# Kernel optimization log

Hardware: AMD Instinct MI355X
Metric: run time of the kernel (lower is better)

Reference implementation:

```python
import jax, jax.numpy as jnp
import numpy as np

K = 3  # Chebyshev filter size (max_view)


def avwgcn(X, E, weights_pool, bias_pool):
    """Adaptive node-wise graph conv. X: [B,N,C_in], E: [N,D]."""
    N = E.shape[0]
    # adaptive adjacency: softmax over rows of relu(E E^T)
    supports = jax.nn.softmax(jax.nn.relu(E @ E.T), axis=1)  # [N,N]
    support_set = [jnp.eye(N, dtype=X.dtype), supports]
    for _ in range(2, K):  # Chebyshev recursion
        support_set.append(2.0 * supports @ support_set[-1] - support_set[-2])
    S = jnp.stack(support_set, axis=0)  # [K,N,N]
    W = jnp.einsum('nd,dkio->nkio', E, weights_pool)  # per-node weights [N,K,Ci,Co]
    bias = E @ bias_pool  # [N,Co]
    XG = jnp.einsum('knm,bmc->bnkc', S, X)  # [B,N,K,Ci]
    return jnp.einsum('bnki,nkio->bno', XG, W) + bias  # [B,N,Co]


def setup_inputs() -> dict:
    key = jax.random.key(0)
    ks = jax.random.split(key, 5)
    B, N, Cin, Cout, D = 32, 4096, 2, 64, 10
    Ci = Cin + Cout  # 66
    X = jax.random.normal(ks[0], (B, N, Cin), dtype=jnp.float32)
    H = jnp.zeros((B, N, Cout), dtype=jnp.float32)
    E = jax.random.normal(ks[1], (N, D), dtype=jnp.float32)
    W_gate = jax.random.normal(ks[2], (D, K, Ci, 2 * Cout), dtype=jnp.float32) * 0.1
    b_gate = jnp.zeros((D, 2 * Cout), dtype=jnp.float32)
    W_update = jax.random.normal(ks[3], (D, K, Ci, Cout), dtype=jnp.float32) * 0.1
    b_update = jnp.zeros((D, Cout), dtype=jnp.float32)
    return {"X": X, "H": H, "E": E, "W_gate": W_gate, "b_gate": b_gate,
            "W_update": W_update, "b_update": b_update}


def reference(X, H, E, W_gate, b_gate, W_update, b_update):
    Cout = H.shape[-1]
    XH = jnp.concatenate([X, H], axis=-1)  # [B,N,Cin+Cout]
    ZR = jax.nn.sigmoid(avwgcn(XH, E, W_gate, b_gate))  # [B,N,2*Cout]
    Z, R = ZR[..., :Cout], ZR[..., Cout:]
    C = jnp.concatenate([X, Z * H], axis=-1)
    HC = jnp.tanh(avwgcn(C, E, W_update, b_update))
    return R * H + (1.0 - R) * HC
```

## Files before the change

### kernel.cpp

```cpp
#include <hip/hip_runtime.h>
#include <math.h>

#define N_NODES 4096
#define BATCH   32
#define D_EMB   10
#define CIN     2
#define COUT    64
#define CI      66
#define KSUP    3
#define NCOLS   2112
#define NPAD    2176
#define LDT     4096

#define KSEC    72
#define KI_REAL 216
#define KILD    232
#define OCH     (32 * KILD)
#define WROW_G  (128 * KILD)
#define WROW_U  (64 * KILD)
#define WGT2_R  (WROW_G + WROW_U)

typedef _Float16 half_t;
typedef __attribute__((ext_vector_type(8))) _Float16 f16x8;
typedef __attribute__((ext_vector_type(4))) _Float16 f16x4;
typedef __attribute__((ext_vector_type(2))) _Float16 f16x2;
typedef __attribute__((ext_vector_type(4))) float f32x4;

union u32h2 { unsigned u; f16x2 h; };

struct __attribute__((packed, aligned(4))) uint4_u4 { uint4 v; };
__device__ __forceinline__ f16x8 loadu8h(const half_t* p) {
  union { uint4 u; f16x8 h; } r;
  r.u = ((const uint4_u4*)p)->v;
  return r.h;
}

__device__ __forceinline__ float fast_sigmoid(float x) { return 1.f / (1.f + __expf(-x)); }
__device__ __forceinline__ float fast_tanh(float x) { return 1.f - 2.f / (__expf(2.f * x) + 1.f); }

__device__ __forceinline__ void gld_lds16(const half_t* g, half_t* l) {
  __builtin_amdgcn_global_load_lds(
      (const __attribute__((address_space(1))) void*)g,
      (__attribute__((address_space(3))) void*)l, 16, 0, 0);
}

__global__ __launch_bounds__(256) void k_softmax_p(const float* __restrict__ E,
                                                   half_t* __restrict__ Pb) {
  const int n = blockIdx.x;
  const int tid = threadIdx.x;
  __shared__ float En[D_EMB];
  __shared__ float ms[256], ss[256];
  if (tid < D_EMB) En[tid] = E[n * D_EMB + tid];
  __syncthreads();
  float en[D_EMB];
#pragma unroll
  for (int d = 0; d < D_EMB; ++d) en[d] = En[d];

  float val[16];
  float m = -1e30f, s = 0.f;
#pragma unroll
  for (int it = 0; it < 16; ++it) {
    const int c = tid + it * 256;
    const float* Ec = E + c * D_EMB;
    float v = 0.f;
#pragma unroll
    for (int d = 0; d < D_EMB; ++d) v += en[d] * Ec[d];
    v = fmaxf(v, 0.f);
    val[it] = v;
    if (v > m) { s *= __expf(m - v); m = v; }
    s += __expf(v - m);
  }
  ms[tid] = m; ss[tid] = s;
  __syncthreads();
  for (int off = 128; off > 0; off >>= 1) {
    if (tid < off) {
      float m2 = ms[tid + off], s2 = ss[tid + off];
      float m1 = ms[tid], s1 = ss[tid];
      float mm = fmaxf(m1, m2);
      ms[tid] = mm;
      ss[tid] = s1 * __expf(m1 - mm) + s2 * __expf(m2 - mm);
    }
    __syncthreads();
  }
  const float M = ms[0];
  const float inv = 1.f / ss[0];
  half_t* Pr = Pb + (size_t)n * N_NODES;
#pragma unroll
  for (int it = 0; it < 16; ++it)
    Pr[tid + it * 256] = (half_t)(__expf(val[it] - M) * inv);
}

__global__ __launch_bounds__(256) void k_build_v0(const float* __restrict__ X,
                                                  const float* __restrict__ H,
                                                  half_t* __restrict__ Vt,
                                                  half_t* __restrict__ Vn,
                                                  half_t* __restrict__ Cbn) {
  __shared__ half_t T[64][69];
  const int tid = threadIdx.x;
  const int ct = blockIdx.x * 64;
  const int mt = blockIdx.y * 64;
  const int r0 = tid >> 4;
  const int c4 = (tid & 15) * 4;
#pragma unroll
  for (int it = 0; it < 4; ++it) {
    const int r = r0 + it * 16;
    const int m = mt + r;
    half_t hv[4];
#pragma unroll
    for (int j = 0; j < 4; ++j) {
      const int col = ct + c4 + j;
      const int b = col / CI;
      const int c = col - b * CI;
      float v;
      if (c < CIN) v = X[((size_t)b * N_NODES + m) * CIN + c];
      else         v = H[((size_t)b * N_NODES + m) * COUT + (c - CIN)];
      hv[j] = (half_t)v;
      T[r][c4 + j] = hv[j];
      if (c < CIN) Cbn[(size_t)m * NPAD + col] = hv[j];
    }
    f16x4 v4 = {hv[0], hv[1], hv[2], hv[3]};
    *(f16x4*)&Vn[(size_t)m * NPAD + ct + c4] = v4;
  }
  __syncthreads();
#pragma unroll
  for (int it = 0; it < 4; ++it) {
    const int cc = r0 + it * 16;
    const int m4 = c4;
    f16x4 v = {T[m4 + 0][cc], T[m4 + 1][cc], T[m4 + 2][cc], T[m4 + 3][cc]};
    *(f16x4*)&Vt[(size_t)(ct + cc) * LDT + mt + m4] = v;
  }
}

__device__ __forceinline__ void gemm_compute_tile(const half_t* __restrict__ Lb,
                                                  int wm, int wn, int fofs,
                                                  f32x4 (&acc)[4][2]) {
  f16x8 a[4], b[2];
#pragma unroll
  for (int i = 0; i < 4; ++i)
    a[i] = *(const f16x8*)&Lb[((wm >> 4) + i) * 512 + fofs];
#pragma unroll
  for (int j = 0; j < 2; ++j)
    b[j] = *(const f16x8*)&Lb[4096 + ((wn >> 4) + j) * 512 + fofs];
  __builtin_amdgcn_s_setprio(1);
#pragma unroll
  for (int i = 0; i < 4; ++i)
#pragma unroll
    for (int j = 0; j < 2; ++j)
      acc[i][j] = __builtin_amdgcn_mfma_f32_16x16x32_f16(a[i], b[j], acc[i][j], 0, 0, 0);
  __builtin_amdgcn_s_setprio(0);
}

__global__ __launch_bounds__(512) void k_gemm_f16(const half_t* __restrict__ A,
                                                  const half_t* __restrict__ Bt,
                                                  half_t* __restrict__ Cn,
                                                  half_t* __restrict__ Ct) {
  __shared__ half_t LB[4][8192];
  const int tid = threadIdx.x;
  const int lane = tid & 63;
  const int wave = tid >> 6;

  int flat = blockIdx.y * 17 + blockIdx.x;
  flat = (flat & 7) * 68 + (flat >> 3);
  const int bx = flat % 17;
  const int by = flat / 17;

  const int wm = (wave >> 2) * 64;
  const int wn = (wave & 3) * 32;
  const int rb = by * 128;
  const int cb = bx * 128;

  const int srow = lane >> 2;
  const int skg = (((lane & 3) + ((lane >> 3) & 3)) & 3) * 8;
  const half_t* ga0 = A + (size_t)(rb + wave * 16 + srow) * N_NODES + skg;
  const half_t* gb0 = Bt + (size_t)(cb + wave * 16 + srow) * LDT + skg;
  const int lA0 = wave * 512;
  const int lB0 = 4096 + wave * 512;

  const int fr = lane & 15;
  const int fg = lane >> 4;
  const int fofs = (4 * fr + ((fg - (fr >> 1)) & 3)) * 8;

  f32x4 acc[4][2] = {};

#define STAGE_T(buf, kk) do { half_t* Lp = LB[(buf)]; \
    gld_lds16(ga0 + (kk), Lp + lA0); gld_lds16(gb0 + (kk), Lp + lB0); } while (0)

  STAGE_T(0, 0);
  STAGE_T(1, 32);
  STAGE_T(2, 64);

  for (int t = 0; t < 124; t += 4) {
    asm volatile("s_waitcnt vmcnt(4)\n\ts_barrier" ::: "memory");
    STAGE_T(3, (t + 3) * 32);
    gemm_compute_tile(LB[0], wm, wn, fofs, acc);

    asm volatile("s_waitcnt vmcnt(4)\n\ts_barrier" ::: "memory");
    STAGE_T(0, (t + 4) * 32);
    gemm_compute_tile(LB[1], wm, wn, fofs, acc);

    asm volatile("s_waitcnt vmcnt(4)\n\ts_barrier" ::: "memory");
    STAGE_T(1, (t + 5) * 32);
    gemm_compute_tile(LB[2], wm, wn, fofs, acc);

    asm volatile("s_waitcnt vmcnt(4)\n\ts_barrier" ::: "memory");
    STAGE_T(2, (t + 6) * 32);
    gemm_compute_tile(LB[3], wm, wn, fofs, acc);
  }
  asm volatile("s_waitcnt vmcnt(4)\n\ts_barrier" ::: "memory");
  STAGE_T(3, 127 * 32);
  gemm_compute_tile(LB[0], wm, wn, fofs, acc);
  asm volatile("s_waitcnt vmcnt(4)\n\ts_barrier" ::: "memory");
  gemm_compute_tile(LB[1], wm, wn, fofs, acc);
  asm volatile("s_waitcnt vmcnt(2)\n\ts_barrier" ::: "memory");
  gemm_compute_tile(LB[2], wm, wn, fofs, acc);
  asm volatile("s_waitcnt vmcnt(0)\n\ts_barrier" ::: "memory");
  gemm_compute_tile(LB[3], wm, wn, fofs, acc);
#undef STAGE_T

  const int en = lane & 15;
  const int em = (lane >> 4) * 4;
#pragma unroll
  for (int i = 0; i < 4; ++i) {
#pragma unroll
    for (int j = 0; j < 2; ++j) {
      const int m0 = rb + wm + i * 16 + em;
      const int n = cb + wn + j * 16 + en;
      half_t h0 = (half_t)acc[i][j][0];
      half_t h1 = (half_t)acc[i][j][1];
      half_t h2 = (half_t)acc[i][j][2];
      half_t h3 = (half_t)acc[i][j][3];
      if (Ct) {
        f16x4 t4 = {h0, h1, h2, h3};
        *(f16x4*)&Ct[(size_t)n * LDT + m0] = t4;
      }
      Cn[(size_t)(m0 + 0) * NPAD + n] = h0;
      Cn[(size_t)(m0 + 1) * NPAD + n] = h1;
      Cn[(size_t)(m0 + 2) * NPAD + n] = h2;
      Cn[(size_t)(m0 + 3) * NPAD + n] = h3;
    }
  }
}

__global__ __launch_bounds__(256) void k_tr(const half_t* __restrict__ Cbn,
                                            half_t* __restrict__ Ct) {
  __shared__ half_t T[64][69];
  const int tid = threadIdx.x;
  const int cb = blockIdx.x * 64;
  const int mb = blockIdx.y * 64;
  const int c4 = (tid & 15) * 4;
  const int r0 = tid >> 4;
#pragma unroll
  for (int it = 0; it < 4; ++it) {
    const int r = r0 + it * 16;
    f16x4 v = *(const f16x4*)&Cbn[(size_t)(mb + r) * NPAD + cb + c4];
    T[r][c4 + 0] = v[0];
    T[r][c4 + 1] = v[1];
    T[r][c4 + 2] = v[2];
    T[r][c4 + 3] = v[3];
  }
  __syncthreads();
#pragma unroll
  for (int it = 0; it < 4; ++it) {
    const int c2 = r0 + it * 16;
    const int m4 = c4;
    f16x4 v = {T[m4 + 0][c2], T[m4 + 1][c2], T[m4 + 2][c2], T[m4 + 3][c2]};
    *(f16x4*)&Ct[(size_t)(cb + c2) * LDT + mb + m4] = v;
  }
}

__global__ __launch_bounds__(256) void k_wgt2(const float* __restrict__ Wg,
                                              const float* __restrict__ Wu,
                                              unsigned* __restrict__ WT2) {
  const int r = blockIdx.x * 256 + threadIdx.x;
  if (r >= WGT2_R) return;
  const float* pool;
  int o, ki, ostr;
  if (r < WROW_G) { o = r / KILD; ki = r % KILD; pool = Wg; ostr = 128; }
  else { int r2 = r - WROW_G; o = r2 / KILD; ki = r2 % KILD; pool = Wu; ostr = 64; }
  const int k = ki / KSEC;
  const int i = ki - k * KSEC;
#pragma unroll
  for (int dp = 0; dp < 5; ++dp) {
    u32h2 v; v.h = f16x2{(half_t)0.f, (half_t)0.f};
    if (ki < KI_REAL && i < CI) {
      v.h[0] = (half_t)pool[(((size_t)(2 * dp) * KSUP + k) * CI + i) * ostr + o];
      v.h[1] = (half_t)pool[(((size_t)(2 * dp + 1) * KSUP + k) * CI + i) * ostr + o];
    }
    WT2[(size_t)dp * WGT2_R + r] = v.u;
  }
}

__device__ __forceinline__ void stage_xg4(const half_t* __restrict__ v0b,
                                          const half_t* __restrict__ g1b,
                                          const half_t* __restrict__ g2b,
                                          half_t* __restrict__ xg,
                                          int n0, int tid, int nthr) {
  for (int w = tid; w < 4 * 288; w += nthr) {
    const int nd = w / 288;
    const int rem = w - nd * 288;
    const int b = rem / 9;
    const int oct = rem - b * 9;
    const size_t src = (size_t)(n0 + nd) * NPAD + b * CI;
    half_t* row = xg + nd * OCH + b * KILD;
    const half_t* pv = v0b + src;
    const half_t* pg1 = g1b + src;
    const half_t* pg2 = g2b + src;
    if (oct < 8) {
      const f16x8 v0 = loadu8h(pv + oct * 8);
      const f16x8 g1 = loadu8h(pg1 + oct * 8);
      const f16x8 g2 = loadu8h(pg2 + oct * 8);
      const f16x8 x2 = g2 + g2 - v0;
      *(f16x8*)&row[oct * 8] = v0;
      *(f16x8*)&row[KSEC + oct * 8] = g1;
      *(f16x8*)&row[2 * KSEC + oct * 8] = x2;
    } else {
      u32h2 tv, tg1, tg2;
      tv.u = *(const unsigned*)(pv + 64);
      tg1.u = *(const unsigned*)(pg1 + 64);
      tg2.u = *(const unsigned*)(pg2 + 64);
      f16x8 v0 = {}, g1 = {}, x2 = {};
      v0[0] = tv.h[0]; v0[1] = tv.h[1];
      g1[0] = tg1.h[0]; g1[1] = tg1.h[1];
      x2[0] = tg2.h[0] + tg2.h[0] - tv.h[0];
      x2[1] = tg2.h[1] + tg2.h[1] - tv.h[1];
      *(f16x8*)&row[64] = v0;
      *(f16x8*)&row[KSEC + 64] = g1;
      *(f16x8*)&row[2 * KSEC + 64] = x2;
    }
  }
  for (int w = tid; w < 4 * 64; w += nthr) {
    const int nd = w >> 6;
    const int z = w & 63;
    const f16x8 zz = {};
    *(f16x8*)&xg[nd * OCH + (z >> 1) * KILD + KI_REAL + (z & 1) * 8] = zz;
  }
}

__global__ __launch_bounds__(512) void k_gate_t(const half_t* __restrict__ Vn,
                                                const half_t* __restrict__ G1n,
                                                const half_t* __restrict__ G2n,
                                                const unsigned* __restrict__ WT2,
                                                const float* __restrict__ E,
                                                const float* __restrict__ bg,
                                                const float* __restrict__ H,
                                                half_t* __restrict__ Cbn,
                                                half_t* __restrict__ Rb) {
  const int n0 = blockIdx.x * 4;
  const int tid = threadIdx.x;
  const int lane = tid & 63;
  const int wave = tid >> 6;
  __shared__ half_t S[4 * OCH];
  __shared__ float biasl[4][128];

  f16x2 e2p[4][5];
#pragma unroll
  for (int nd = 0; nd < 4; ++nd)
#pragma unroll
    for (int dp = 0; dp < 5; ++dp) {
      e2p[nd][dp][0] = (half_t)E[(n0 + nd) * D_EMB + 2 * dp];
      e2p[nd][dp][1] = (half_t)E[(n0 + nd) * D_EMB + 2 * dp + 1];
    }

  {
    const int nn = tid >> 7;
    const int o = tid & 127;
    float s = 0.f;
#pragma unroll
    for (int d = 0; d < D_EMB; ++d) s += E[(n0 + nn) * D_EMB + d] * bg[d * 128 + o];
    biasl[nn][o] = s;
  }
  stage_xg4(Vn, G1n, G2n, S, n0, tid, 512);
  __syncthreads();

  const int fr = lane & 15;
  const int fk = (lane >> 4) * 8;
  const int en = lane & 15;
  const int em = (lane >> 4) * 4;
  const int node = wave & 3;
  const int bh = wave >> 2;
  const int nn = n0 + node;

  f16x8 af[7];
#pragma unroll
  for (int ks = 0; ks < 7; ++ks)
    af[ks] = *(const f16x8*)&S[node * OCH + (bh * 16 + fr) * KILD + ks * 32 + fk];
  __syncthreads();

#pragma unroll
  for (int p = 0; p < 4; ++p) {
    if (p > 0) __syncthreads();
    for (int base = tid * 8; base < OCH; base += 4096) {
      float a[4][8] = {};
#pragma unroll
      for (int dp = 0; dp < 5; ++dp) {
        const unsigned* wrow = WT2 + (size_t)dp * WGT2_R + p * OCH + base;
        uint4 wa = *(const uint4*)wrow;
        uint4 wb = *(const uint4*)(wrow + 4);
        u32h2 c0, c1, c2, c3;
        c0.u = wa.x; c1.u = wa.y; c2.u = wa.z; c3.u = wa.w;
#pragma unroll
        for (int nd = 0; nd < 4; ++nd) {
          a[nd][0] = __builtin_amdgcn_fdot2(c0.h, e2p[nd][dp], a[nd][0], false);
          a[nd][1] = __builtin_amdgcn_fdot2(c1.h, e2p[nd][dp], a[nd][1], false);
          a[nd][2] = __builtin_amdgcn_fdot2(c2.h, e2p[nd][dp], a[nd][2], false);
          a[nd][3] = __builtin_amdgcn_fdot2(c3.h, e2p[nd][dp], a[nd][3], false);
        }
        c0.u = wb.x; c1.u = wb.y; c2.u = wb.z; c3.u = wb.w;
#pragma unroll
        for (int nd = 0; nd < 4; ++nd) {
          a[nd][4] = __builtin_amdgcn_fdot2(c0.h, e2p[nd][dp], a[nd][4], false);
          a[nd][5] = __builtin_amdgcn_fdot2(c1.h, e2p[nd][dp], a[nd][5], false);
          a[nd][6] = __builtin_amdgcn_fdot2(c2.h, e2p[nd][dp], a[nd][6], false);
          a[nd][7] = __builtin_amdgcn_fdot2(c3.h, e2p[nd][dp], a[nd][7], false);
        }
      }
#pragma unroll
      for (int nd = 0; nd < 4; ++nd) {
        f16x8 w0;
#pragma unroll
        for (int e = 0; e < 8; ++e) w0[e] = (half_t)a[nd][e];
        *(f16x8*)&S[nd * OCH + base] = w0;
      }
    }
    __syncthreads();

    f32x4 acc2[2] = {};
#pragma unroll
    for (int ks = 0; ks < 7; ++ks) {
#pragma unroll
      for (int ot = 0; ot < 2; ++ot) {
        const f16x8 b0 = *(const f16x8*)&S[node * OCH + (ot * 16 + fr) * KILD + ks * 32 + fk];
        acc2[ot] = __builtin_amdgcn_mfma_f32_16x16x32_f16(af[ks], b0, acc2[ot], 0, 0, 0);
      }
    }
#pragma unroll
    for (int ot = 0; ot < 2; ++ot) {
      const int o_g = p * 32 + ot * 16 + en;
      const float bo = biasl[node][o_g];
#pragma unroll
      for (int r = 0; r < 4; ++r) {
        const int b = bh * 16 + em + r;
        const float s = fast_sigmoid(acc2[ot][r] + bo);
        if (p < 2) {
          const float hv = H[((size_t)b * N_NODES + nn) * COUT + o_g];
          const half_t z = (half_t)(s * hv);
          Cbn[(size_t)nn * NPAD + b * CI + CIN + o_g] = z;
        } else {
          Rb[(size_t)nn * 2048 + b * COUT + (o_g - 64)] = (half_t)s;
        }
      }
    }
  }
}

__global__ __launch_bounds__(512) void k_update_t(const half_t* __restrict__ Cbn,
                                                  const half_t* __restrict__ G1n,
                                                  const half_t* __restrict__ G2n,
                                                  const unsigned* __restrict__ WT2,
                                                  const float* __restrict__ E,
                                                  const float* __restrict__ bu,
                                                  const float* __restrict__ H,
                                                  const half_t* __restrict__ Rb,
                                                  float* __restrict__ Out) {
  const int n0 = blockIdx.x * 4;
  const int tid = threadIdx.x;
  const int lane = tid & 63;
  const int wave = tid >> 6;
  __shared__ half_t S[4 * OCH];
  __shared__ float biasl[4][64];

  f16x2 e2p[4][5];
#pragma unroll
  for (int nd = 0; nd < 4; ++nd)
#pragma unroll
    for (int dp = 0; dp < 5; ++dp) {
      e2p[nd][dp][0] = (half_t)E[(n0 + nd) * D_EMB + 2 * dp];
      e2p[nd][dp][1] = (half_t)E[(n0 + nd) * D_EMB + 2 * dp + 1];
    }

  if (tid < 256) {
    const int nn = tid >> 6;
    const int o = tid & 63;
    float s = 0.f;
#pragma unroll
    for (int d = 0; d < D_EMB; ++d) s += E[(n0 + nn) * D_EMB + d] * bu[d * COUT + o];
    biasl[nn][o] = s;
  }
  stage_xg4(Cbn, G1n, G2n, S, n0, tid, 512);
  __syncthreads();

  const int fr = lane & 15;
  const int fk = (lane >> 4) * 8;
  const int en = lane & 15;
  const int em = (lane >> 4) * 4;
  const int node = wave & 3;
  const int bh = wave >> 2;
  const int nn = n0 + node;

  f16x8 af[7];
#pragma unroll
  for (int ks = 0; ks < 7; ++ks)
    af[ks] = *(const f16x8*)&S[node * OCH + (bh * 16 + fr) * KILD + ks * 32 + fk];
  __syncthreads();

#pragma unroll
  for (int p = 0; p < 2; ++p) {
    if (p > 0) __syncthreads();
    for (int base = tid * 8; base < OCH; base += 4096) {
      float a[4][8] = {};
#pragma unroll
      for (int dp = 0; dp < 5; ++dp) {
        const unsigned* wrow = WT2 + (size_t)dp * WGT2_R + WROW_G + p * OCH + base;
        uint4 wa = *(const uint4*)wrow;
        uint4 wb = *(const uint4*)(wrow + 4);
        u32h2 c0, c1, c2, c3;
        c0.u = wa.x; c1.u = wa.y; c2.u = wa.z; c3.u = wa.w;
#pragma unroll
        for (int nd = 0; nd < 4; ++nd) {
          a[nd][0] = __builtin_amdgcn_fdot2(c0.h, e2p[nd][dp], a[nd][0], false);
          a[nd][1] = __builtin_amdgcn_fdot2(c1.h, e2p[nd][dp], a[nd][1], false);
          a[nd][2] = __builtin_amdgcn_fdot2(c2.h, e2p[nd][dp], a[nd][2], false);
          a[nd][3] = __builtin_amdgcn_fdot2(c3.h, e2p[nd][dp], a[nd][3], false);
        }
        c0.u = wb.x; c1.u = wb.y; c2.u = wb.z; c3.u = wb.w;
#pragma unroll
        for (int nd = 0; nd < 4; ++nd) {
          a[nd][4] = __builtin_amdgcn_fdot2(c0.h, e2p[nd][dp], a[nd][4], false);
          a[nd][5] = __builtin_amdgcn_fdot2(c1.h, e2p[nd][dp], a[nd][5], false);
          a[nd][6] = __builtin_amdgcn_fdot2(c2.h, e2p[nd][dp], a[nd][6], false);
          a[nd][7] = __builtin_amdgcn_fdot2(c3.h, e2p[nd][dp], a[nd][7], false);
        }
      }
#pragma unroll
      for (int nd = 0; nd < 4; ++nd) {
        f16x8 w0;
#pragma unroll
        for (int e = 0; e < 8; ++e) w0[e] = (half_t)a[nd][e];
        *(f16x8*)&S[nd * OCH + base] = w0;
      }
    }
    __syncthreads();

    f32x4 acc2[2] = {};
#pragma unroll
    for (int ks = 0; ks < 7; ++ks) {
#pragma unroll
      for (int ot = 0; ot < 2; ++ot) {
        const f16x8 b0 = *(const f16x8*)&S[node * OCH + (ot * 16 + fr) * KILD + ks * 32 + fk];
        acc2[ot] = __builtin_amdgcn_mfma_f32_16x16x32_f16(af[ks], b0, acc2[ot], 0, 0, 0);
      }
    }
#pragma unroll
    for (int ot = 0; ot < 2; ++ot) {
      const int o = p * 32 + ot * 16 + en;
      const float bo = biasl[node][o];
#pragma unroll
      for (int r = 0; r < 4; ++r) {
        const int b = bh * 16 + em + r;
        const float hc = fast_tanh(acc2[ot][r] + bo);
        const float hv = H[((size_t)b * N_NODES + nn) * COUT + o];
        const float rr = (float)Rb[(size_t)nn * 2048 + b * COUT + o];
        Out[((size_t)b * N_NODES + nn) * COUT + o] = rr * hv + (1.f - rr) * hc;
      }
    }
  }
}

extern "C" void kernel_launch(void* const* d_in, const int* in_sizes, int n_in,
                              void* d_out, int out_size, void* d_ws, size_t ws_size,
                              hipStream_t stream) {
  const float* X  = (const float*)d_in[0];
  const float* H  = (const float*)d_in[1];
  const float* E  = (const float*)d_in[2];
  const float* Wg = (const float*)d_in[3];
  const float* bg = (const float*)d_in[4];
  const float* Wu = (const float*)d_in[5];
  const float* bu = (const float*)d_in[6];
  float* out = (float*)d_out;

  const size_t SZ_P = (size_t)N_NODES * N_NODES;
  const size_t SZ_M = (size_t)NPAD * LDT;
  half_t* Pb  = (half_t*)d_ws;
  half_t* Vt  = Pb + SZ_P;
  half_t* Vn  = Vt + SZ_M;
  half_t* G1t = Vn + SZ_M;
  half_t* G1n = G1t + SZ_M;
  half_t* G2n = G1n + SZ_M;
  half_t* Cbt = G2n + SZ_M;
  half_t* Cbn = Cbt + SZ_M;
  half_t* Rb  = Cbn + SZ_M;
  unsigned* WT2 = (unsigned*)(Rb + (size_t)BATCH * N_NODES * COUT);

  const dim3 gg(17, 32);
  const dim3 gt(33, 64);

  k_softmax_p<<<N_NODES, 256, 0, stream>>>(E, Pb);
  k_build_v0<<<gt, 256, 0, stream>>>(X, H, Vt, Vn, Cbn);
  k_wgt2<<<(WGT2_R + 255) / 256, 256, 0, stream>>>(Wg, Wu, WT2);

  k_gemm_f16<<<gg, 512, 0, stream>>>(Pb, Vt, G1n, G1t);
  k_gemm_f16<<<gg, 512, 0, stream>>>(Pb, G1t, G2n, nullptr);
  k_gate_t<<<N_NODES / 4, 512, 0, stream>>>(Vn, G1n, G2n, WT2, E, bg, H, Cbn, Rb);
  k_tr<<<gt, 256, 0, stream>>>(Cbn, Cbt);

  k_gemm_f16<<<gg, 512, 0, stream>>>(Pb, Cbt, G1n, G1t);
  k_gemm_f16<<<gg, 512, 0, stream>>>(Pb, G1t, G2n, nullptr);
  k_update_t<<<N_NODES / 4, 512, 0, stream>>>(Cbn, G1n, G2n, WT2, E, bu, H, Rb, out);
}
```

Measured before the change: 672.2 us.

## Split K across wave halves with 64x64 warp tiles and LDS reduction in GEMM

```diff
diff --git a/kernel.cpp b/kernel.cpp
--- a/kernel.cpp
+++ b/kernel.cpp
@@ -131,30 +131,11 @@
   }
 }
 
-__device__ __forceinline__ void gemm_compute_tile(const half_t* __restrict__ Lb,
-                                                  int wm, int wn, int fofs,
-                                                  f32x4 (&acc)[4][2]) {
-  f16x8 a[4], b[2];
-#pragma unroll
-  for (int i = 0; i < 4; ++i)
-    a[i] = *(const f16x8*)&Lb[((wm >> 4) + i) * 512 + fofs];
-#pragma unroll
-  for (int j = 0; j < 2; ++j)
-    b[j] = *(const f16x8*)&Lb[4096 + ((wn >> 4) + j) * 512 + fofs];
-  __builtin_amdgcn_s_setprio(1);
-#pragma unroll
-  for (int i = 0; i < 4; ++i)
-#pragma unroll
-    for (int j = 0; j < 2; ++j)
-      acc[i][j] = __builtin_amdgcn_mfma_f32_16x16x32_f16(a[i], b[j], acc[i][j], 0, 0, 0);
-  __builtin_amdgcn_s_setprio(0);
-}
-
 __global__ __launch_bounds__(512) void k_gemm_f16(const half_t* __restrict__ A,
                                                   const half_t* __restrict__ Bt,
                                                   half_t* __restrict__ Cn,
                                                   half_t* __restrict__ Ct) {
-  __shared__ half_t LB[4][8192];
+  __shared__ half_t LB[2][16384];
   const int tid = threadIdx.x;
   const int lane = tid & 63;
   const int wave = tid >> 6;
@@ -164,8 +145,10 @@
   const int bx = flat % 17;
   const int by = flat / 17;
 
-  const int wm = (wave >> 2) * 64;
-  const int wn = (wave & 3) * 32;
+  const int quad = wave & 3;
+  const int kh = wave >> 2;
+  const int wm = (quad >> 1) * 64;
+  const int wn = (quad & 1) * 64;
   const int rb = by * 128;
   const int cb = bx * 128;
 
@@ -174,69 +157,86 @@
   const half_t* ga0 = A + (size_t)(rb + wave * 16 + srow) * N_NODES + skg;
   const half_t* gb0 = Bt + (size_t)(cb + wave * 16 + srow) * LDT + skg;
   const int lA0 = wave * 512;
-  const int lB0 = 4096 + wave * 512;
+  const int lA1 = 4096 + wave * 512;
+  const int lB0 = 8192 + wave * 512;
+  const int lB1 = 12288 + wave * 512;
 
   const int fr = lane & 15;
   const int fg = lane >> 4;
   const int fofs = (4 * fr + ((fg - (fr >> 1)) & 3)) * 8;
 
-  f32x4 acc[4][2] = {};
+  const int aBase = kh * 4096 + (wm >> 4) * 512 + fofs;
+  const int bBase = 8192 + kh * 4096 + (wn >> 4) * 512 + fofs;
+
+  f32x4 acc[4][4] = {};
 
 #define STAGE_T(buf, kk) do { half_t* Lp = LB[(buf)]; \
-    gld_lds16(ga0 + (kk), Lp + lA0); gld_lds16(gb0 + (kk), Lp + lB0); } while (0)
+    gld_lds16(ga0 + (kk), Lp + lA0); gld_lds16(ga0 + (kk) + 32, Lp + lA1); \
+    gld_lds16(gb0 + (kk), Lp + lB0); gld_lds16(gb0 + (kk) + 32, Lp + lB1); } while (0)
+
+#define COMPUTE_T(buf) do { const half_t* Lp = LB[(buf)]; \
+    f16x8 af[4], bf[4]; \
+    _Pragma("unroll") for (int i = 0; i < 4; ++i) af[i] = *(const f16x8*)&Lp[aBase + i * 512]; \
+    _Pragma("unroll") for (int j = 0; j < 4; ++j) bf[j] = *(const f16x8*)&Lp[bBase + j * 512]; \
+    __builtin_amdgcn_s_setprio(1); \
+    _Pragma("unroll") for (int i = 0; i < 4; ++i) \
+      _Pragma("unroll") for (int j = 0; j < 4; ++j) \
+        acc[i][j] = __builtin_amdgcn_mfma_f32_16x16x32_f16(af[i], bf[j], acc[i][j], 0, 0, 0); \
+    __builtin_amdgcn_s_setprio(0); } while (0)
 
   STAGE_T(0, 0);
-  STAGE_T(1, 32);
-  STAGE_T(2, 64);
-
-  for (int t = 0; t < 124; t += 4) {
-    asm volatile("s_waitcnt vmcnt(4)\n\ts_barrier" ::: "memory");
-    STAGE_T(3, (t + 3) * 32);
-    gemm_compute_tile(LB[0], wm, wn, fofs, acc);
-
-    asm volatile("s_waitcnt vmcnt(4)\n\ts_barrier" ::: "memory");
-    STAGE_T(0, (t + 4) * 32);
-    gemm_compute_tile(LB[1], wm, wn, fofs, acc);
-
-    asm volatile("s_waitcnt vmcnt(4)\n\ts_barrier" ::: "memory");
-    STAGE_T(1, (t + 5) * 32);
-    gemm_compute_tile(LB[2], wm, wn, fofs, acc);
-
-    asm volatile("s_waitcnt vmcnt(4)\n\ts_barrier" ::: "memory");
-    STAGE_T(2, (t + 6) * 32);
-    gemm_compute_tile(LB[3], wm, wn, fofs, acc);
-  }
-  asm volatile("s_waitcnt vmcnt(4)\n\ts_barrier" ::: "memory");
-  STAGE_T(3, 127 * 32);
-  gemm_compute_tile(LB[0], wm, wn, fofs, acc);
-  asm volatile("s_waitcnt vmcnt(4)\n\ts_barrier" ::: "memory");
-  gemm_compute_tile(LB[1], wm, wn, fofs, acc);
-  asm volatile("s_waitcnt vmcnt(2)\n\ts_barrier" ::: "memory");
-  gemm_compute_tile(LB[2], wm, wn, fofs, acc);
+
+  for (int t = 0; t < 62; t += 2) {
+    asm volatile("s_waitcnt vmcnt(0)\n\ts_barrier" ::: "memory");
+    STAGE_T(1, (t + 1) * 64);
+    COMPUTE_T(0);
+
+    asm volatile("s_waitcnt vmcnt(0)\n\ts_barrier" ::: "memory");
+    STAGE_T(0, (t + 2) * 64);
+    COMPUTE_T(1);
+  }
   asm volatile("s_waitcnt vmcnt(0)\n\ts_barrier" ::: "memory");
-  gemm_compute_tile(LB[3], wm, wn, fofs, acc);
+  STAGE_T(1, 63 * 64);
+  COMPUTE_T(0);
+  asm volatile("s_waitcnt vmcnt(0)\n\ts_barrier" ::: "memory");
+  COMPUTE_T(1);
 #undef STAGE_T
-
-  const int en = lane & 15;
-  const int em = (lane >> 4) * 4;
-#pragma unroll
-  for (int i = 0; i < 4; ++i) {
-#pragma unroll
-    for (int j = 0; j < 2; ++j) {
-      const int m0 = rb + wm + i * 16 + em;
-      const int n = cb + wn + j * 16 + en;
-      half_t h0 = (half_t)acc[i][j][0];
-      half_t h1 = (half_t)acc[i][j][1];
-      half_t h2 = (half_t)acc[i][j][2];
-      half_t h3 = (half_t)acc[i][j][3];
-      if (Ct) {
-        f16x4 t4 = {h0, h1, h2, h3};
-        *(f16x4*)&Ct[(size_t)n * LDT + m0] = t4;
-      }
-      Cn[(size_t)(m0 + 0) * NPAD + n] = h0;
-      Cn[(size_t)(m0 + 1) * NPAD + n] = h1;
-      Cn[(size_t)(m0 + 2) * NPAD + n] = h2;
-      Cn[(size_t)(m0 + 3) * NPAD + n] = h3;
+#undef COMPUTE_T
+
+  __syncthreads();
+  float* Lf = (float*)LB;
+  if (kh == 1) {
+#pragma unroll
+    for (int i = 0; i < 4; ++i)
+#pragma unroll
+      for (int j = 0; j < 4; ++j)
+        *(f32x4*)&Lf[quad * 4096 + (i * 4 + j) * 256 + lane * 4] = acc[i][j];
+  }
+  __syncthreads();
+  if (kh == 0) {
+    const int en = lane & 15;
+    const int em = (lane >> 4) * 4;
+#pragma unroll
+    for (int i = 0; i < 4; ++i) {
+#pragma unroll
+      for (int j = 0; j < 4; ++j) {
+        const f32x4 pr = *(const f32x4*)&Lf[quad * 4096 + (i * 4 + j) * 256 + lane * 4];
+        const f32x4 s4 = acc[i][j] + pr;
+        const int m0 = rb + wm + i * 16 + em;
+        const int n = cb + wn + j * 16 + en;
+        half_t h0 = (half_t)s4[0];
+        half_t h1 = (half_t)s4[1];
+        half_t h2 = (half_t)s4[2];
+        half_t h3 = (half_t)s4[3];
+        if (Ct) {
+          f16x4 t4 = {h0, h1, h2, h3};
+          *(f16x4*)&Ct[(size_t)n * LDT + m0] = t4;
+        }
+        Cn[(size_t)(m0 + 0) * NPAD + n] = h0;
+        Cn[(size_t)(m0 + 1) * NPAD + n] = h1;
+        Cn[(size_t)(m0 + 2) * NPAD + n] = h2;
+        Cn[(size_t)(m0 + 3) * NPAD + n] = h3;
+      }
     }
   }
 }
```

New measurement: 782.2 us. 1.16x slower.
